# Optimization experiments

Measured on AMD Instinct MI355X. Metric: run time of the kernel, lower is better.

## Reference

```python
import jax, jax.numpy as jnp
import numpy as np

DIM = 128   # EMBED_DIM
NH = 4      # N_HEADS
HD = DIM // NH          # 32
NT = max(1, int(NH * 0.25))  # 1 timelike head
NS = NH - NT                 # 3 spacelike heads
TD = NT * HD                 # T_DIM = 32
SD = 6      # STATE_DIM
TIN, TOUT = 20, 20
NL = 3      # N_LAYERS
B, T = 4096, TIN + TOUT      # seq len capped by pos embedding (40)


def _ln(x, g, b):
    m = jnp.mean(x, -1, keepdims=True)
    v = jnp.mean((x - m) ** 2, -1, keepdims=True)
    return g * (x - m) * jax.lax.rsqrt(v + 1e-5) + b


def _mln(x, pg, pb, g, b):
    # MinkowskiLN: standard LN then scale by |sum(s^2)-sum(t^2)| norm
    x = _ln(x, pg, pb)
    t = x[..., :TD]
    s = x[..., TD:]
    mq = jnp.sum(s * s, -1, keepdims=True) - jnp.sum(t * t, -1, keepdims=True)
    eps = jnp.maximum(0.01 * jnp.mean(jnp.abs(mq)), 1e-5)
    return g * (x / (jnp.sqrt(jnp.abs(mq) + eps) + eps)) + b


def _attn(h, qt, kt, qs, ks, vw, ow, ob, ws):
    # Minkowski attention (mode='f3'): timelike scores negated with learned sigmoid weight
    Bb, Tt, _ = h.shape
    scale = HD ** -0.5
    Qt = (h @ qt).reshape(Bb, Tt, NT, HD)
    Kt = (h @ kt).reshape(Bb, Tt, NT, HD)
    Qs = (h @ qs).reshape(Bb, Tt, NS, HD)
    Ks = (h @ ks).reshape(Bb, Tt, NS, HD)
    st = jnp.einsum('bthd,bshd->bths', Qt, Kt)  # [B,T,NT,T]
    ss = jnp.einsum('bthd,bshd->bths', Qs, Ks)  # [B,T,NS,T]
    score = jnp.concatenate([-jax.nn.sigmoid(ws) * st, ss], axis=2) * scale
    a = jax.nn.softmax(score, axis=-1)
    V = (h @ vw).reshape(Bb, Tt, NH, HD)
    o = jnp.einsum('bths,bshd->bthd', a, V).reshape(Bb, Tt, DIM)
    return o @ ow + ob


def setup_inputs() -> dict:
    key = jax.random.key(0)
    ks = iter(jax.random.split(key, 32))
    def w(shape, s=0.02):
        return (jax.random.normal(next(ks), shape, jnp.float32) * s).astype(jnp.float32)
    inp = {
        'x': jax.random.normal(next(ks), (B, T, SD), jnp.float32),
        'embed_w': w((SD, DIM)), 'embed_b': jnp.zeros((DIM,), jnp.float32),
        'pos': w((TIN + TOUT, DIM)),
        'qt_w': w((NL, DIM, NT * HD)), 'kt_w': w((NL, DIM, NT * HD)),
        'qs_w': w((NL, DIM, NS * HD)), 'ks_w': w((NL, DIM, NS * HD)),
        'v_w': w((NL, DIM, DIM)), 'out_w': w((NL, DIM, DIM)), 'out_b': jnp.zeros((NL, DIM), jnp.float32),
        'w_sigma': jnp.zeros((NL,), jnp.float32),
        'n1_pre_g': jnp.ones((NL, DIM), jnp.float32), 'n1_pre_b': jnp.zeros((NL, DIM), jnp.float32),
        'n1_g': jnp.ones((NL, DIM), jnp.float32), 'n1_b': jnp.zeros((NL, DIM), jnp.float32),
        'n2_pre_g': jnp.ones((NL, DIM), jnp.float32), 'n2_pre_b': jnp.zeros((NL, DIM), jnp.float32),
        'n2_g': jnp.ones((NL, DIM), jnp.float32), 'n2_b': jnp.zeros((NL, DIM), jnp.float32),
        'ff_w1': w((NL, DIM, 4 * DIM)), 'ff_b1': jnp.zeros((NL, 4 * DIM), jnp.float32),
        'ff_w2': w((NL, 4 * DIM, DIM)), 'ff_b2': jnp.zeros((NL, DIM), jnp.float32),
        'fn_pre_g': jnp.ones((DIM,), jnp.float32), 'fn_pre_b': jnp.zeros((DIM,), jnp.float32),
        'fn_g': jnp.ones((DIM,), jnp.float32), 'fn_b': jnp.zeros((DIM,), jnp.float32),
        'traj_w': w((DIM, SD * TOUT)), 'traj_b': jnp.zeros((SD * TOUT,), jnp.float32),
    }
    return inp


def reference(x, embed_w, embed_b, pos, qt_w, kt_w, qs_w, ks_w, v_w, out_w, out_b,
              w_sigma, n1_pre_g, n1_pre_b, n1_g, n1_b, n2_pre_g, n2_pre_b, n2_g, n2_b,
              ff_w1, ff_b1, ff_w2, ff_b2, fn_pre_g, fn_pre_b, fn_g, fn_b, traj_w, traj_b):
    Tt = x.shape[1]
    h = x @ embed_w + embed_b + pos[:Tt]  # [B,T,D]
    for i in range(NL):
        h = h + _attn(_mln(h, n1_pre_g[i], n1_pre_b[i], n1_g[i], n1_b[i]),
                      qt_w[i], kt_w[i], qs_w[i], ks_w[i], v_w[i], out_w[i], out_b[i], w_sigma[i])
        hn = _mln(h, n2_pre_g[i], n2_pre_b[i], n2_g[i], n2_b[i])
        h = h + (jax.nn.gelu(hn @ ff_w1[i] + ff_b1[i], approximate=False) @ ff_w2[i] + ff_b2[i])
    h = _mln(h, fn_pre_g, fn_pre_b, fn_g, fn_b)[:, -1, :]  # [B,D]
    out = h @ traj_w + traj_b
    return out.reshape(x.shape[0], TOUT, SD)
```

## Files before the change

### kernel.cpp

```cpp
#include <hip/hip_runtime.h>
#include <hip/hip_bf16.h>

#define DIMM 128
#define TT   40
#define BB   4096
#define NTOK (BB*TT)
#define NLAY 3

typedef float f4 __attribute__((ext_vector_type(4)));
typedef float f32x4 __attribute__((ext_vector_type(4)));
typedef short bf16x8 __attribute__((ext_vector_type(8)));

__device__ __forceinline__ float bf2f(unsigned short u) {
    union { unsigned int i; float f; } v; v.i = ((unsigned int)u) << 16; return v.f;
}
__device__ __forceinline__ unsigned short f2bu(float f) {
    __hip_bfloat16 h = __float2bfloat16(f);
    return *reinterpret_cast<unsigned short*>(&h);
}
__device__ __forceinline__ float gelu_f(float v) {
    float z = 1.5957691216057308f * fmaf(0.044715f * v * v, v, v);
    return v / (1.f + __expf(-z));
}

__device__ __forceinline__ void mln_rowstat(
    const float* v, const float* pgv, const float* pbv,
    float& m, float& rstd, float& mq)
{
    float s1 = 0.f, s2 = 0.f;
    #pragma unroll
    for (int nf = 0; nf < 8; ++nf) { s1 += v[nf]; s2 += v[nf]*v[nf]; }
    #pragma unroll
    for (int o = 1; o < 16; o <<= 1) { s1 += __shfl_xor(s1, o); s2 += __shfl_xor(s2, o); }
    m = s1 * (1.f/128.f);
    float var = s2 * (1.f/128.f) - m*m;
    rstd = rsqrtf(fmaxf(var, 0.f) + 1e-5f);
    float q = 0.f;
    #pragma unroll
    for (int nf = 0; nf < 8; ++nf) {
        float yv = (v[nf] - m) * rstd * pgv[nf] + pbv[nf];
        q += (nf < 2 ? -(yv*yv) : (yv*yv));
    }
    #pragma unroll
    for (int o = 1; o < 16; o <<= 1) q += __shfl_xor(q, o);
    mq = q;
}

__device__ __forceinline__ void build_mln_frags1(
    bf16x8 a[4], const float* __restrict__ h, int row,
    const float* __restrict__ stats, float eps,
    const float* __restrict__ pg, const float* __restrict__ pb,
    const float* __restrict__ gg, const float* __restrict__ gb, int q)
{
    float m  = stats[(size_t)row*4 + 0];
    float rs = stats[(size_t)row*4 + 1];
    float mq = stats[(size_t)row*4 + 2];
    float s3 = 1.f / (sqrtf(fabsf(mq) + eps) + eps);
    float rss3 = rs * s3, mm = -m * rss3;
    #pragma unroll
    for (int ks = 0; ks < 4; ++ks) {
        int c0 = ks*32 + q*8;
        f4 x0 = *(const f4*)(h + (size_t)row*128 + c0);
        f4 x1 = *(const f4*)(h + (size_t)row*128 + c0 + 4);
        union { unsigned short u[8]; bf16x8 v; } o;
        #pragma unroll
        for (int j = 0; j < 4; ++j) {
            float g0 = gg[c0+j], g1 = gg[c0+j+4];
            float t0 = fmaf(x0[j], rss3, mm);
            float t1 = fmaf(x1[j], rss3, mm);
            o.u[j]   = f2bu(fmaf(g0 * pg[c0+j],   t0, fmaf(g0 * pb[c0+j],   s3, gb[c0+j])));
            o.u[j+4] = f2bu(fmaf(g1 * pg[c0+j+4], t1, fmaf(g1 * pb[c0+j+4], s3, gb[c0+j+4])));
        }
        a[ks] = o.v;
    }
}

__global__ __launch_bounds__(256) void pack_w_k(
    const float* __restrict__ qt, const float* __restrict__ kt,
    const float* __restrict__ qs, const float* __restrict__ ks,
    const float* __restrict__ vw, const float* __restrict__ ow,
    const float* __restrict__ w1, const float* __restrict__ w2,
    unsigned short* __restrict__ wqT, unsigned short* __restrict__ outT,
    unsigned short* __restrict__ ff1T, unsigned short* __restrict__ ff2T)
{
    int idx = blockIdx.x * 256 + threadIdx.x;
    if (idx < 147456) {
        int i = idx / 49152, r = idx % 49152;
        int n = r / 128, k = r % 128;
        float v;
        if (n < 32)        v = qt[i*4096  + k*32  + n];
        else if (n < 64)   v = kt[i*4096  + k*32  + (n-32)];
        else if (n < 160)  v = qs[i*12288 + k*96  + (n-64)];
        else if (n < 256)  v = ks[i*12288 + k*96  + (n-160)];
        else               v = vw[i*16384 + k*128 + (n-256)];
        wqT[idx] = f2bu(v);
    } else if (idx < 196608) {
        int j = idx - 147456;
        int i = j / 16384, r = j % 16384;
        int n = r / 128, k = r % 128;
        outT[j] = f2bu(ow[i*16384 + k*128 + n]);
    } else if (idx < 393216) {
        int j = idx - 196608;
        int i = j / 65536, r = j % 65536;
        int n = r / 128, k = r % 128;
        ff1T[j] = f2bu(w1[i*65536 + k*512 + n]);
    } else {
        int j = idx - 393216;
        int i = j / 65536, r = j % 65536;
        int n = r / 512, k = r % 512;
        ff2T[j] = f2bu(w2[i*65536 + k*128 + n]);
    }
}

__global__ __launch_bounds__(256) void embed_stats_k(
    const float* __restrict__ x, const float* __restrict__ ew,
    const float* __restrict__ eb, const float* __restrict__ pos,
    const float* __restrict__ pg, const float* __restrict__ pb,
    float* __restrict__ h, float* __restrict__ stats, float* __restrict__ partials)
{
    int wid = threadIdx.x >> 6, lane = threadIdx.x & 63;
    int tok = blockIdx.x * 4 + wid;
    int t = tok % TT;
    const float* xr = x + (size_t)tok * 6;
    float xv[6];
    #pragma unroll
    for (int k = 0; k < 6; ++k) xv[k] = xr[k];
    int d0 = lane, d1 = lane + 64;
    float x0 = eb[d0] + pos[t*128 + d0];
    float x1 = eb[d1] + pos[t*128 + d1];
    #pragma unroll
    for (int k = 0; k < 6; ++k) {
        x0 += xv[k] * ew[k*128 + d0];
        x1 += xv[k] * ew[k*128 + d1];
    }
    h[(size_t)tok*128 + d0] = x0;
    h[(size_t)tok*128 + d1] = x1;

    float s = x0 + x1;
    #pragma unroll
    for (int o = 32; o > 0; o >>= 1) s += __shfl_xor(s, o);
    float m = s * (1.f / 128.f);
    float e0 = x0 - m, e1 = x1 - m;
    float v = e0*e0 + e1*e1;
    #pragma unroll
    for (int o = 32; o > 0; o >>= 1) v += __shfl_xor(v, o);
    float rstd = rsqrtf(v * (1.f / 128.f) + 1e-5f);
    float y0 = e0 * rstd * pg[lane]      + pb[lane];
    float y1 = e1 * rstd * pg[lane + 64] + pb[lane + 64];
    float q = (lane < 32 ? -(y0*y0) : (y0*y0)) + y1*y1;
    #pragma unroll
    for (int o = 32; o > 0; o >>= 1) q += __shfl_xor(q, o);
    if (lane == 0) {
        stats[(size_t)tok*4 + 0] = m;
        stats[(size_t)tok*4 + 1] = rstd;
        stats[(size_t)tok*4 + 2] = q;
    }
    __shared__ float pm[4];
    if (lane == 0) pm[wid] = fabsf(q);
    __syncthreads();
    if (threadIdx.x == 0) partials[blockIdx.x] = (pm[0] + pm[1]) + (pm[2] + pm[3]);
}

__global__ __launch_bounds__(1024) void reduce_eps_k(
    const float* __restrict__ partials, int n, float* __restrict__ scal)
{
    float s = 0.f;
    for (int i = threadIdx.x; i < n; i += 1024) s += partials[i];
    __shared__ float sm[1024];
    sm[threadIdx.x] = s;
    __syncthreads();
    for (int o = 512; o > 0; o >>= 1) {
        if (threadIdx.x < o) sm[threadIdx.x] += sm[threadIdx.x + o];
        __syncthreads();
    }
    if (threadIdx.x == 0) {
        float mean = sm[0] / (float)NTOK;
        scal[0] = fmaxf(0.01f * mean, 1e-5f);
    }
}

__global__ __launch_bounds__(512) void qkv_k(
    const float* __restrict__ hsrc,
    const float* __restrict__ stats_in, const float* __restrict__ scal,
    const float* __restrict__ pg, const float* __restrict__ pb,
    const float* __restrict__ gg, const float* __restrict__ gb,
    const unsigned short* __restrict__ BT,
    unsigned short* __restrict__ obuf)
{
    __shared__ unsigned char Wl[32768];
    const int tid = threadIdx.x, wid = tid >> 6, lane = tid & 63;
    const int q = lane >> 4, l15 = lane & 15;
    const int row0 = blockIdx.x * 128;
    const int wrow = row0 + wid * 16;

    bf16x8 a[4];
    build_mln_frags1(a, hsrc, wrow + l15,
                     stats_in, scal[0], pg, pb, gg, gb, q);

    const unsigned char* BTb = (const unsigned char*)BT;
    for (int nc = 0; nc < 3; ++nc) {
        __syncthreads();
        {
            int row = tid >> 2, seg = tid & 3;
            #pragma unroll
            for (int jj = 0; jj < 4; ++jj) {
                int colb = seg*64 + jj*16;
                uint4 v = *(const uint4*)(BTb + (size_t)(nc*128 + row)*256 + colb);
                *(uint4*)(Wl + row*256 + (colb ^ ((row & 7) << 4))) = v;
            }
        }
        __syncthreads();
        f32x4 acc[8] = {};
        #pragma unroll
        for (int ks = 0; ks < 4; ++ks)
            #pragma unroll
            for (int nf = 0; nf < 8; ++nf) {
                int row = nf*16 + l15;
                bf16x8 b = *(const bf16x8*)(Wl + row*256 + ((ks*64 + q*16) ^ ((row & 7) << 4)));
                acc[nf] = __builtin_amdgcn_mfma_f32_16x16x32_bf16(a[ks], b, acc[nf], 0, 0, 0);
            }
        #pragma unroll
        for (int r = 0; r < 4; ++r) {
            int row = wrow + q*4 + r;
            #pragma unroll
            for (int nf = 0; nf < 8; ++nf)
                obuf[(size_t)row*384 + nc*128 + nf*16 + l15] = f2bu(acc[nf][r]);
        }
    }
}

__global__ __launch_bounds__(256) void attn_k(
    const unsigned short* __restrict__ scratch, const float* __restrict__ wsp,
    const unsigned short* __restrict__ outT,
    const float* __restrict__ bias,
    float* __restrict__ hres,
    const float* __restrict__ pre_g, const float* __restrict__ pre_b,
    float* __restrict__ stats, float* __restrict__ partials)
{
    __shared__ unsigned char lds[45056];
    __shared__ float sm[16];
    const int b = blockIdx.x, tid = threadIdx.x;
    const unsigned short* base = scratch + (size_t)b * TT * 384;

    unsigned char* VtL = lds;
    unsigned char* PlL = lds + 16384;

    for (int e = tid; e < 1536; e += 256) {
        int hh = e / 384, rem = e - hh*384;
        int row = rem >> 3, c = rem & 7;
        int byte = hh*6144 + ((row*128 + 96 + 4*c) ^ ((row & 7) << 4));
        *(unsigned int*)(PlL + byte) = 0u;
    }
    for (int e = tid; e < 1536; e += 256) {
        int hh = e / 384, rem = e - hh*384;
        int d = rem / 12, sc2 = rem - d*12;
        int s = 40 + 2*sc2;
        int byte = hh*4096 + ((d*128 + s*2) ^ (((d >> 3) & 7) << 4));
        *(unsigned int*)(VtL + byte) = 0u;
    }
    for (int e = tid; e < 640; e += 256) {
        int s = e >> 4, ck = e & 15;
        union { bf16x8 v; unsigned short u[8]; } g;
        g.v = *(const bf16x8*)(base + (size_t)s*384 + 256 + ck*8);
        int hh = ck >> 2, d0 = (ck & 3) * 8;
        #pragma unroll
        for (int j = 0; j < 8; ++j) {
            int d = d0 + j;
            int byte = hh*4096 + ((d*128 + s*2) ^ (((d >> 3) & 7) << 4));
            *(unsigned short*)(VtL + byte) = g.u[j];
        }
    }
    __syncthreads();

    const int h = tid >> 6, lane = tid & 63;
    const int l15 = lane & 15, q4 = lane >> 4;
    const unsigned char* Vt = VtL + h*4096;
    unsigned char* Pl = PlL + h*6144;

    const int qcol = (h == 0) ? 0  : 32  + h*32;
    const int kcol = (h == 0) ? 32 : 128 + h*32;
    const float scale = 0.17677669529663687f;
    const float wmul = (h == 0) ? (-scale / (1.f + __expf(-wsp[0]))) : scale;

    bf16x8 aq[3], bk[3];
    #pragma unroll
    for (int mt = 0; mt < 3; ++mt) {
        int t = l15 + 16*mt; if (t > 39) t = 39;
        aq[mt] = *(const bf16x8*)(base + (size_t)t*384 + qcol + q4*8);
    }
    #pragma unroll
    for (int jt = 0; jt < 3; ++jt) {
        int s = l15 + 16*jt; if (s > 39) s = 39;
        bk[jt] = *(const bf16x8*)(base + (size_t)s*384 + kcol + q4*8);
    }
    f32x4 sc[3][3] = {};
    #pragma unroll
    for (int mt = 0; mt < 3; ++mt)
        #pragma unroll
        for (int jt = 0; jt < 3; ++jt)
            sc[mt][jt] = __builtin_amdgcn_mfma_f32_16x16x32_bf16(aq[mt], bk[jt], sc[mt][jt], 0, 0, 0);

    const bool mask2 = (l15 >= 8);
    float inv[3][4];
    #pragma unroll
    for (int mt = 0; mt < 3; ++mt) {
        #pragma unroll
        for (int r = 0; r < 4; ++r) {
            float s0 = wmul * sc[mt][0][r];
            float s1 = wmul * sc[mt][1][r];
            float s2 = mask2 ? -1e30f : wmul * sc[mt][2][r];
            float mx = fmaxf(fmaxf(s0, s1), s2);
            #pragma unroll
            for (int o = 1; o < 16; o <<= 1) mx = fmaxf(mx, __shfl_xor(mx, o));
            float e0 = __expf(s0 - mx), e1 = __expf(s1 - mx), e2 = __expf(s2 - mx);
            float sum = e0 + e1 + e2;
            #pragma unroll
            for (int o = 1; o < 16; o <<= 1) sum += __shfl_xor(sum, o);
            inv[mt][r] = 1.f / sum;
            int row = 16*mt + 4*q4 + r;
            int rsw = (row & 7) << 4;
            *(unsigned short*)(Pl + ((row*128 + l15*2       ) ^ rsw)) = f2bu(e0);
            *(unsigned short*)(Pl + ((row*128 + 32 + l15*2  ) ^ rsw)) = f2bu(e1);
            *(unsigned short*)(Pl + ((row*128 + 64 + l15*2  ) ^ rsw)) = f2bu(e2);
        }
    }

    f32x4 oacc[3][2] = {};
    #pragma unroll
    for (int ks2 = 0; ks2 < 2; ++ks2) {
        bf16x8 bv[2];
        #pragma unroll
        for (int nt = 0; nt < 2; ++nt) {
            int d = l15 + 16*nt;
            bv[nt] = *(const bf16x8*)(Vt + ((d*128 + 64*ks2 + 16*q4) ^ (((d >> 3) & 7) << 4)));
        }
        #pragma unroll
        for (int mt = 0; mt < 3; ++mt) {
            int row = l15 + 16*mt;
            bf16x8 pa = *(const bf16x8*)(Pl + ((row*128 + 64*ks2 + 16*q4) ^ ((row & 7) << 4)));
            #pragma unroll
            for (int nt = 0; nt < 2; ++nt)
                oacc[mt][nt] = __builtin_amdgcn_mfma_f32_16x16x32_bf16(pa, bv[nt], oacc[mt][nt], 0, 0, 0);
        }
    }

    __syncthreads();
    unsigned char* Ol = lds;
    unsigned char* Wl = lds + 12288;

    #pragma unroll
    for (int mt = 0; mt < 3; ++mt) {
        #pragma unroll
        for (int r = 0; r < 4; ++r) {
            int row = 16*mt + 4*q4 + r;
            float iv = inv[mt][r];
            int rsw = (row & 7) << 4;
            #pragma unroll
            for (int nt = 0; nt < 2; ++nt) {
                int colb = (h*32 + nt*16 + l15) * 2;
                *(unsigned short*)(Ol + ((row*256 + colb) ^ rsw)) = f2bu(oacc[mt][nt][r] * iv);
            }
        }
    }
    {
        const unsigned char* BTb = (const unsigned char*)outT;
        int row = tid >> 1, half = tid & 1;
        #pragma unroll
        for (int jj = 0; jj < 8; ++jj) {
            int colb = half*128 + jj*16;
            uint4 v = *(const uint4*)(BTb + (size_t)row*256 + colb);
            *(uint4*)(Wl + row*256 + (colb ^ ((row & 7) << 4))) = v;
        }
    }
    if (h == 3 && l15 == 0) sm[12 + q4] = 0.f;
    __syncthreads();

    if (h < 3) {
        int arow = 16*h + l15;
        bf16x8 ao[4];
        #pragma unroll
        for (int ks = 0; ks < 4; ++ks)
            ao[ks] = *(const bf16x8*)(Ol + arow*256 + ((ks*64 + q4*16) ^ ((arow & 7) << 4)));
        f32x4 oc[8] = {};
        #pragma unroll
        for (int ks = 0; ks < 4; ++ks)
            #pragma unroll
            for (int nf = 0; nf < 8; ++nf) {
                int brow = nf*16 + l15;
                bf16x8 bo = *(const bf16x8*)(Wl + brow*256 + ((ks*64 + q4*16) ^ ((brow & 7) << 4)));
                oc[nf] = __builtin_amdgcn_mfma_f32_16x16x32_bf16(ao[ks], bo, oc[nf], 0, 0, 0);
            }

        float bv[8], pgv[8], pbv[8];
        #pragma unroll
        for (int nf = 0; nf < 8; ++nf) {
            int c = nf*16 + l15;
            bv[nf] = bias[c]; pgv[nf] = pre_g[c]; pbv[nf] = pre_b[c];
        }
        float amq = 0.f;
        #pragma unroll
        for (int r = 0; r < 4; ++r) {
            int t = 16*h + 4*q4 + r;
            if (t < 40) {
                int row = b*TT + t;
                float* hr = hres + (size_t)row*128;
                float v[8];
                #pragma unroll
                for (int nf = 0; nf < 8; ++nf) {
                    float hv = hr[nf*16 + l15] + oc[nf][r] + bv[nf];
                    hr[nf*16 + l15] = hv;
                    v[nf] = hv;
                }
                float m, rstd, mq;
                mln_rowstat(v, pgv, pbv, m, rstd, mq);
                if (l15 == 0) {
                    stats[(size_t)row*4 + 0] = m;
                    stats[(size_t)row*4 + 1] = rstd;
                    stats[(size_t)row*4 + 2] = mq;
                }
                amq += fabsf(mq);
            }
        }
        if (l15 == 0) sm[h*4 + q4] = amq;
    }
    __syncthreads();
    if (tid == 0) {
        float s = 0.f;
        #pragma unroll
        for (int j = 0; j < 16; ++j) s += sm[j];
        partials[b] = s;
    }
}

__global__ __launch_bounds__(512) void ffn_k(
    const float* __restrict__ hsrc,
    const float* __restrict__ stats_in, const float* __restrict__ scal,
    const float* __restrict__ m2_pre_g, const float* __restrict__ m2_pre_b,
    const float* __restrict__ m2_g, const float* __restrict__ m2_b,
    const unsigned short* __restrict__ W1T,
    const float* __restrict__ b1,
    const unsigned short* __restrict__ W2T,
    const float* __restrict__ b2,
    float* __restrict__ h,
    const float* __restrict__ pre_g, const float* __restrict__ pre_b,
    float* __restrict__ stats, float* __restrict__ partials)
{
    __shared__ unsigned char W1l[16384];
    __shared__ unsigned char W2l[16384];
    __shared__ unsigned char Ps[8][16*144];
    __shared__ float sm[32];
    const int tid = threadIdx.x, wid = tid >> 6, lane = tid & 63;
    const int q = lane >> 4, l15 = lane & 15;
    const int row0 = blockIdx.x * 128;
    const int wrow = row0 + wid * 16;
    unsigned char* Pw = Ps[wid];

    bf16x8 a[4];
    build_mln_frags1(a, hsrc, wrow + l15,
                     stats_in, scal[0], m2_pre_g, m2_pre_b, m2_g, m2_b, q);

    float b2v[8];
    #pragma unroll
    for (int nf = 0; nf < 8; ++nf) b2v[nf] = b2[nf*16 + l15];

    f32x4 acc2[8] = {};
    const unsigned char* W1b = (const unsigned char*)W1T;
    const unsigned char* W2b = (const unsigned char*)W2T;

    for (int c = 0; c < 8; ++c) {
        __syncthreads();
        {
            int row = tid >> 3, seg = tid & 7;
            #pragma unroll
            for (int jj = 0; jj < 2; ++jj) {
                int colb = seg*32 + jj*16;
                uint4 v = *(const uint4*)(W1b + (size_t)(c*64 + row)*256 + colb);
                *(uint4*)(W1l + row*256 + (colb ^ ((row & 7) << 4))) = v;
            }
        }
        {
            int row = tid >> 2, seg = tid & 3;
            #pragma unroll
            for (int jj = 0; jj < 2; ++jj) {
                int colb = seg*32 + jj*16;
                uint4 v = *(const uint4*)(W2b + (size_t)row*1024 + c*128 + colb);
                *(uint4*)(W2l + row*128 + (colb ^ ((row & 7) << 4))) = v;
            }
        }
        __syncthreads();
        float bbv[4];
        #pragma unroll
        for (int nf = 0; nf < 4; ++nf) bbv[nf] = b1[c*64 + nf*16 + l15];
        f32x4 acc1[4];
        #pragma unroll
        for (int nf = 0; nf < 4; ++nf)
            acc1[nf] = f32x4{bbv[nf], bbv[nf], bbv[nf], bbv[nf]};
        #pragma unroll
        for (int ks = 0; ks < 4; ++ks)
            #pragma unroll
            for (int nf = 0; nf < 4; ++nf) {
                int row = nf*16 + l15;
                bf16x8 b = *(const bf16x8*)(W1l + row*256 + ((ks*64 + q*16) ^ ((row & 7) << 4)));
                acc1[nf] = __builtin_amdgcn_mfma_f32_16x16x32_bf16(a[ks], b, acc1[nf], 0, 0, 0);
            }
        #pragma unroll
        for (int nf = 0; nf < 4; ++nf) {
            #pragma unroll
            for (int r = 0; r < 4; ++r) {
                float v = gelu_f(acc1[nf][r]);
                *(unsigned short*)(Pw + (q*4 + r)*144 + (nf*16 + l15)*2) = f2bu(v);
            }
        }
        #pragma unroll
        for (int ks2 = 0; ks2 < 2; ++ks2) {
            bf16x8 a2 = *(const bf16x8*)(Pw + l15*144 + ks2*64 + q*16);
            #pragma unroll
            for (int nf = 0; nf < 8; ++nf) {
                int row = nf*16 + l15;
                bf16x8 b = *(const bf16x8*)(W2l + row*128 + ((ks2*64 + q*16) ^ ((row & 7) << 4)));
                acc2[nf] = __builtin_amdgcn_mfma_f32_16x16x32_bf16(a2, b, acc2[nf], 0, 0, 0);
            }
        }
    }

    float pgv[8], pbv[8];
    #pragma unroll
    for (int nf = 0; nf < 8; ++nf) { pgv[nf] = pre_g[nf*16 + l15]; pbv[nf] = pre_b[nf*16 + l15]; }
    float amq = 0.f;
    #pragma unroll
    for (int r = 0; r < 4; ++r) {
        int row = wrow + q*4 + r;
        float* hr = h + (size_t)row*128;
        float v[8];
        #pragma unroll
        for (int nf = 0; nf < 8; ++nf) {
            float hv = hr[nf*16 + l15] + acc2[nf][r] + b2v[nf];
            hr[nf*16 + l15] = hv;
            v[nf] = hv;
        }
        float m, rstd, mq;
        mln_rowstat(v, pgv, pbv, m, rstd, mq);
        if (l15 == 0) {
            stats[(size_t)row*4 + 0] = m;
            stats[(size_t)row*4 + 1] = rstd;
            stats[(size_t)row*4 + 2] = mq;
        }
        amq += fabsf(mq);
    }
    if (l15 == 0) sm[wid*4 + q] = amq;
    __syncthreads();
    if (tid == 0) {
        float s = 0.f;
        #pragma unroll
        for (int j = 0; j < 32; ++j) s += sm[j];
        partials[blockIdx.x] = s;
    }
}

__global__ __launch_bounds__(128) void head_k(
    const float* __restrict__ h, const float* __restrict__ stats, const float* __restrict__ scal,
    const float* __restrict__ pg, const float* __restrict__ pb,
    const float* __restrict__ gg, const float* __restrict__ gb,
    const float* __restrict__ tw, const float* __restrict__ tb,
    float* __restrict__ out)
{
    int b = blockIdx.x, tid = threadIdx.x;
    int tok = b*TT + (TT - 1);
    __shared__ float ys[128];
    float eps = scal[0];
    float m  = stats[(size_t)tok*4 + 0];
    float rs = stats[(size_t)tok*4 + 1];
    float mq = stats[(size_t)tok*4 + 2];
    float s3 = 1.f / (sqrtf(fabsf(mq) + eps) + eps);
    float x = h[(size_t)tok*128 + tid];
    ys[tid] = gg[tid] * (((x - m) * rs * pg[tid] + pb[tid]) * s3) + gb[tid];
    __syncthreads();
    if (tid < 120) {
        float acc = tb[tid];
        #pragma unroll 4
        for (int d = 0; d < 128; ++d) acc += ys[d] * tw[d*120 + tid];
        out[(size_t)b*120 + tid] = acc;
    }
}

extern "C" void kernel_launch(void* const* d_in, const int* in_sizes, int n_in,
                              void* d_out, int out_size, void* d_ws, size_t ws_size,
                              hipStream_t stream) {
    const float* x        = (const float*)d_in[0];
    const float* embed_w  = (const float*)d_in[1];
    const float* embed_b  = (const float*)d_in[2];
    const float* pos      = (const float*)d_in[3];
    const float* qt_w     = (const float*)d_in[4];
    const float* kt_w     = (const float*)d_in[5];
    const float* qs_w     = (const float*)d_in[6];
    const float* ks_w     = (const float*)d_in[7];
    const float* v_w      = (const float*)d_in[8];
    const float* out_w    = (const float*)d_in[9];
    const float* out_b    = (const float*)d_in[10];
    const float* w_sigma  = (const float*)d_in[11];
    const float* n1_pre_g = (const float*)d_in[12];
    const float* n1_pre_b = (const float*)d_in[13];
    const float* n1_g     = (const float*)d_in[14];
    const float* n1_b     = (const float*)d_in[15];
    const float* n2_pre_g = (const float*)d_in[16];
    const float* n2_pre_b = (const float*)d_in[17];
    const float* n2_g     = (const float*)d_in[18];
    const float* n2_b     = (const float*)d_in[19];
    const float* ff_w1    = (const float*)d_in[20];
    const float* ff_b1    = (const float*)d_in[21];
    const float* ff_w2    = (const float*)d_in[22];
    const float* ff_b2    = (const float*)d_in[23];
    const float* fn_pre_g = (const float*)d_in[24];
    const float* fn_pre_b = (const float*)d_in[25];
    const float* fn_g     = (const float*)d_in[26];
    const float* fn_b     = (const float*)d_in[27];
    const float* traj_w   = (const float*)d_in[28];
    const float* traj_b   = (const float*)d_in[29];

    char* ws = (char*)d_ws;
    float*          h        = (float*)ws;
    float*          stats    = (float*)(ws + 83886080);
    unsigned short* scratch  = (unsigned short*)(ws + 86507520);
    unsigned short* wqT      = (unsigned short*)(ws + 212336640);
    unsigned short* outT     = (unsigned short*)(ws + 212631552);
    unsigned short* ff1T     = (unsigned short*)(ws + 212729856);
    unsigned short* ff2T     = (unsigned short*)(ws + 213123072);
    float*          partials = (float*)(ws + 213516288);
    float*          scal     = (float*)(ws + 213680128);

    pack_w_k<<<2304, 256, 0, stream>>>(qt_w, kt_w, qs_w, ks_w, v_w, out_w, ff_w1, ff_w2,
                                       wqT, outT, ff1T, ff2T);
    embed_stats_k<<<40960, 256, 0, stream>>>(x, embed_w, embed_b, pos,
                                             n1_pre_g, n1_pre_b, h, stats, partials);
    reduce_eps_k<<<1, 1024, 0, stream>>>(partials, 40960, scal);

    for (int i = 0; i < NLAY; ++i) {
        qkv_k<<<1280, 512, 0, stream>>>(
            h, stats, scal,
            n1_pre_g + i*128, n1_pre_b + i*128, n1_g + i*128, n1_b + i*128,
            wqT + (size_t)i*49152, scratch);
        attn_k<<<4096, 256, 0, stream>>>(
            scratch, w_sigma + i,
            outT + (size_t)i*16384, out_b + i*128,
            h, n2_pre_g + i*128, n2_pre_b + i*128,
            stats, partials);
        reduce_eps_k<<<1, 1024, 0, stream>>>(partials, 4096, scal);
        const float* npg = (i < NLAY-1) ? (n1_pre_g + (i+1)*128) : fn_pre_g;
        const float* npb = (i < NLAY-1) ? (n1_pre_b + (i+1)*128) : fn_pre_b;
        ffn_k<<<1280, 512, 0, stream>>>(
            h, stats, scal,
            n2_pre_g + i*128, n2_pre_b + i*128, n2_g + i*128, n2_b + i*128,
            ff1T + (size_t)i*65536, ff_b1 + i*512,
            ff2T + (size_t)i*65536, ff_b2 + i*128, h,
            npg, npb, stats, partials);
        reduce_eps_k<<<1, 1024, 0, stream>>>(partials, 1280, scal);
    }

    head_k<<<4096, 128, 0, stream>>>(h, stats, scal, fn_pre_g, fn_pre_b, fn_g, fn_b,
                                     traj_w, traj_b, (float*)d_out);
}
```

Baseline: 842.8 us.

## Fuse QKV projection into attention kernel, keep QKV in LDS

Merges the QKV projection kernel into the attention kernel. Each block now computes the MinkowskiLN fragments and the QKV GEMM for its own batch element (40 tokens), stages the result in padded LDS, and no longer writes it to and reads it back from a global scratch buffer. This removes one launch and the bf16 QKV round trip through HBM, roughly 126MB of traffic each way per layer. In exchange, LDS use per block grows to about 77KB, which lowers occupancy. The QKV weights are also reloaded per 40-token block instead of per 128-row block, and the 40 rows are padded to 48 for the MFMA tiles.

```diff
diff --git a/kernel.cpp b/kernel.cpp
--- a/kernel.cpp
+++ b/kernel.cpp
@@ -179,71 +179,72 @@
     }
 }
 
-__global__ __launch_bounds__(512) void qkv_k(
+__global__ __launch_bounds__(256) void qkvattn_k(
     const float* __restrict__ hsrc,
     const float* __restrict__ stats_in, const float* __restrict__ scal,
     const float* __restrict__ pg, const float* __restrict__ pb,
     const float* __restrict__ gg, const float* __restrict__ gb,
     const unsigned short* __restrict__ BT,
-    unsigned short* __restrict__ obuf)
-{
-    __shared__ unsigned char Wl[32768];
-    const int tid = threadIdx.x, wid = tid >> 6, lane = tid & 63;
-    const int q = lane >> 4, l15 = lane & 15;
-    const int row0 = blockIdx.x * 128;
-    const int wrow = row0 + wid * 16;
-
-    bf16x8 a[4];
-    build_mln_frags1(a, hsrc, wrow + l15,
-                     stats_in, scal[0], pg, pb, gg, gb, q);
-
-    const unsigned char* BTb = (const unsigned char*)BT;
-    for (int nc = 0; nc < 3; ++nc) {
-        __syncthreads();
-        {
-            int row = tid >> 2, seg = tid & 3;
-            #pragma unroll
-            for (int jj = 0; jj < 4; ++jj) {
-                int colb = seg*64 + jj*16;
-                uint4 v = *(const uint4*)(BTb + (size_t)(nc*128 + row)*256 + colb);
-                *(uint4*)(Wl + row*256 + (colb ^ ((row & 7) << 4))) = v;
-            }
-        }
-        __syncthreads();
-        f32x4 acc[8] = {};
-        #pragma unroll
-        for (int ks = 0; ks < 4; ++ks)
-            #pragma unroll
-            for (int nf = 0; nf < 8; ++nf) {
-                int row = nf*16 + l15;
-                bf16x8 b = *(const bf16x8*)(Wl + row*256 + ((ks*64 + q*16) ^ ((row & 7) << 4)));
-                acc[nf] = __builtin_amdgcn_mfma_f32_16x16x32_bf16(a[ks], b, acc[nf], 0, 0, 0);
-            }
-        #pragma unroll
-        for (int r = 0; r < 4; ++r) {
-            int row = wrow + q*4 + r;
-            #pragma unroll
-            for (int nf = 0; nf < 8; ++nf)
-                obuf[(size_t)row*384 + nc*128 + nf*16 + l15] = f2bu(acc[nf][r]);
-        }
-    }
-}
-
-__global__ __launch_bounds__(256) void attn_k(
-    const unsigned short* __restrict__ scratch, const float* __restrict__ wsp,
+    const float* __restrict__ wsp,
     const unsigned short* __restrict__ outT,
     const float* __restrict__ bias,
     float* __restrict__ hres,
     const float* __restrict__ pre_g, const float* __restrict__ pre_b,
     float* __restrict__ stats, float* __restrict__ partials)
 {
-    __shared__ unsigned char lds[45056];
+    __shared__ unsigned char lds[78592];
     __shared__ float sm[16];
     const int b = blockIdx.x, tid = threadIdx.x;
-    const unsigned short* base = scratch + (size_t)b * TT * 384;
+    const int wid = tid >> 6, lane = tid & 63;
+    const int q4 = lane >> 4, l15 = lane & 15;
 
     unsigned char* VtL = lds;
     unsigned char* PlL = lds + 16384;
+    unsigned short* qkvL = (unsigned short*)(lds + 40960);
+    unsigned char* WqC = lds;
+
+    bf16x8 a[3][4];
+    #pragma unroll
+    for (int mt = 0; mt < 3; ++mt) {
+        int t0 = 16*mt + l15; if (t0 > 39) t0 = 39;
+        build_mln_frags1(a[mt], hsrc, b*TT + t0, stats_in, scal[0], pg, pb, gg, gb, q4);
+    }
+    const unsigned char* BTb = (const unsigned char*)BT;
+    for (int nc = 0; nc < 3; ++nc) {
+        __syncthreads();
+        {
+            int row = tid >> 1, half = tid & 1;
+            #pragma unroll
+            for (int jj = 0; jj < 8; ++jj) {
+                int colb = half*128 + jj*16;
+                uint4 v = *(const uint4*)(BTb + (size_t)(nc*128 + row)*256 + colb);
+                *(uint4*)(WqC + row*256 + (colb ^ ((row & 7) << 4))) = v;
+            }
+        }
+        __syncthreads();
+        f32x4 acc[3][2] = {};
+        #pragma unroll
+        for (int ks = 0; ks < 4; ++ks)
+            #pragma unroll
+            for (int nf2 = 0; nf2 < 2; ++nf2) {
+                int row = (wid*2 + nf2)*16 + l15;
+                bf16x8 bfr = *(const bf16x8*)(WqC + row*256 + ((ks*64 + q4*16) ^ ((row & 7) << 4)));
+                #pragma unroll
+                for (int mt = 0; mt < 3; ++mt)
+                    acc[mt][nf2] = __builtin_amdgcn_mfma_f32_16x16x32_bf16(a[mt][ks], bfr, acc[mt][nf2], 0, 0, 0);
+            }
+        #pragma unroll
+        for (int mt = 0; mt < 3; ++mt)
+            #pragma unroll
+            for (int nf2 = 0; nf2 < 2; ++nf2)
+                #pragma unroll
+                for (int r = 0; r < 4; ++r) {
+                    int row = 16*mt + 4*q4 + r;
+                    int col = nc*128 + (wid*2 + nf2)*16 + l15;
+                    qkvL[(size_t)row*392 + col] = f2bu(acc[mt][nf2][r]);
+                }
+    }
+    __syncthreads();
 
     for (int e = tid; e < 1536; e += 256) {
         int hh = e / 384, rem = e - hh*384;
@@ -261,7 +262,7 @@
     for (int e = tid; e < 640; e += 256) {
         int s = e >> 4, ck = e & 15;
         union { bf16x8 v; unsigned short u[8]; } g;
-        g.v = *(const bf16x8*)(base + (size_t)s*384 + 256 + ck*8);
+        g.v = *(const bf16x8*)(qkvL + (size_t)s*392 + 256 + ck*8);
         int hh = ck >> 2, d0 = (ck & 3) * 8;
         #pragma unroll
         for (int j = 0; j < 8; ++j) {
@@ -272,8 +273,7 @@
     }
     __syncthreads();
 
-    const int h = tid >> 6, lane = tid & 63;
-    const int l15 = lane & 15, q4 = lane >> 4;
+    const int h = tid >> 6;
     const unsigned char* Vt = VtL + h*4096;
     unsigned char* Pl = PlL + h*6144;
 
@@ -286,12 +286,12 @@
     #pragma unroll
     for (int mt = 0; mt < 3; ++mt) {
         int t = l15 + 16*mt; if (t > 39) t = 39;
-        aq[mt] = *(const bf16x8*)(base + (size_t)t*384 + qcol + q4*8);
+        aq[mt] = *(const bf16x8*)(qkvL + (size_t)t*392 + qcol + q4*8);
     }
     #pragma unroll
     for (int jt = 0; jt < 3; ++jt) {
         int s = l15 + 16*jt; if (s > 39) s = 39;
-        bk[jt] = *(const bf16x8*)(base + (size_t)s*384 + kcol + q4*8);
+        bk[jt] = *(const bf16x8*)(qkvL + (size_t)s*392 + kcol + q4*8);
     }
     f32x4 sc[3][3] = {};
     #pragma unroll
@@ -363,12 +363,12 @@
         }
     }
     {
-        const unsigned char* BTb = (const unsigned char*)outT;
+        const unsigned char* BTo = (const unsigned char*)outT;
         int row = tid >> 1, half = tid & 1;
         #pragma unroll
         for (int jj = 0; jj < 8; ++jj) {
             int colb = half*128 + jj*16;
-            uint4 v = *(const uint4*)(BTb + (size_t)row*256 + colb);
+            uint4 v = *(const uint4*)(BTo + (size_t)row*256 + colb);
             *(uint4*)(Wl + row*256 + (colb ^ ((row & 7) << 4))) = v;
         }
     }
@@ -620,7 +620,6 @@
     char* ws = (char*)d_ws;
     float*          h        = (float*)ws;
     float*          stats    = (float*)(ws + 83886080);
-    unsigned short* scratch  = (unsigned short*)(ws + 86507520);
     unsigned short* wqT      = (unsigned short*)(ws + 212336640);
     unsigned short* outT     = (unsigned short*)(ws + 212631552);
     unsigned short* ff1T     = (unsigned short*)(ws + 212729856);
@@ -635,12 +634,11 @@
     reduce_eps_k<<<1, 1024, 0, stream>>>(partials, 40960, scal);
 
     for (int i = 0; i < NLAY; ++i) {
-        qkv_k<<<1280, 512, 0, stream>>>(
+        qkvattn_k<<<4096, 256, 0, stream>>>(
             h, stats, scal,
             n1_pre_g + i*128, n1_pre_b + i*128, n1_g + i*128, n1_b + i*128,
-            wqT + (size_t)i*49152, scratch);
-        attn_k<<<4096, 256, 0, stream>>>(
-            scratch, w_sigma + i,
+            wqT + (size_t)i*49152,
+            w_sigma + i,
             outT + (size_t)i*16384, out_b + i*128,
             h, n2_pre_g + i*128, n2_pre_b + i*128,
             stats, partials);
```

New measurement: 923.5 us. 9.6% more time.
